# Performance work log

Hardware: AMD Instinct MI355X
Metric: run time of the kernel (lower is better)

Reference implementation:

```python
import jax, jax.numpy as jnp
import numpy as np

N = 4096
N_FEAT = 1024
N_HID = 8
N_HEADS = 8
N_CLASSES = 16
ALPHA = 0.2
NEG_BIG = -9e15


def setup_inputs() -> dict:
    key = jax.random.key(0)
    ks = jax.random.split(key, 6)
    x = jax.random.normal(ks[0], (N, N_FEAT), dtype=jnp.float32)
    adj = (jax.random.uniform(ks[1], (N, N)) < 0.01).astype(jnp.float32)
    adj = jnp.maximum(adj, jnp.eye(N, dtype=jnp.float32))
    W_heads = jax.random.normal(ks[2], (N_HEADS, N_FEAT, N_HID), dtype=jnp.float32) * 0.05
    a_heads = jax.random.normal(ks[3], (N_HEADS, 2 * N_HID, 1), dtype=jnp.float32) * 0.05
    W_final = jax.random.normal(ks[4], (N_HEADS * N_HID, N_CLASSES), dtype=jnp.float32) * 0.05
    a_final = jax.random.normal(ks[5], (2 * N_CLASSES, 1), dtype=jnp.float32) * 0.05
    return {"x": x, "adj": adj, "W_heads": W_heads, "a_heads": a_heads,
            "W_final": W_final, "a_final": a_final}


def gat_layer(h, adj, W, a):
    # h: [N, Fin], W: [Fin, Fout], a: [2*Fout, 1]
    Wh = h @ W                                  # [N, Fout]
    Fout = W.shape[1]
    f_src = Wh @ a[:Fout, 0]                    # [N] -- Wh_i . a[:F]
    f_dst = Wh @ a[Fout:, 0]                    # [N] -- Wh_j . a[F:]
    e = jax.nn.leaky_relu(f_src[:, None] + f_dst[None, :], ALPHA)  # [N, N]
    e = jnp.where(adj > 0, e, NEG_BIG)
    attention = jax.nn.softmax(e, axis=1)       # dropout skipped (eval mode)
    return attention @ Wh                        # [N, Fout]


def reference(x, adj, W_heads, a_heads, W_final, a_final):
    # multi-head GAT layer (8 independent heads), concat along features
    heads = jax.vmap(lambda W, a: gat_layer(x, adj, W, a))(W_heads, a_heads)  # [H, N, n_hid]
    h = jnp.transpose(heads, (1, 0, 2)).reshape(x.shape[0], -1)               # [N, H*n_hid]
    h = jax.nn.elu(h)
    out = gat_layer(h, adj, W_final, a_final)    # [N, n_classes]
    return jax.nn.log_softmax(out, axis=1)
```

## Files before the change

kernel.cpp:

```cpp
#include <hip/hip_runtime.h>
#include <math.h>

#define N 4096
#define NFEAT 1024
#define NHID 8
#define NHEADS 8
#define NCLS 16
#define CAP 128

#define GEMM_BLOCKS 512

__global__ __launch_bounds__(256) void ka_scan_gemm(const float* __restrict__ adj,
                                                    const float* __restrict__ x,
                                                    const float* __restrict__ W_heads,
                                                    const float* __restrict__ a_heads,
                                                    int* __restrict__ deg,
                                                    int* __restrict__ nbr,
                                                    float* __restrict__ Wh,
                                                    float* __restrict__ fsrc,
                                                    float* __restrict__ fdst) {
    __shared__ float smem[8 * NFEAT + 4 * 8 * 64];
    const int tid = threadIdx.x;

    if (blockIdx.x >= GEMM_BLOCKS) {
        const int row = blockIdx.x - GEMM_BLOCKS;
        int* cnt = (int*)smem;
        if (tid == 0) *cnt = 0;
        __syncthreads();
        const float4* arow = (const float4*)(adj + (size_t)row * N);
        int* outl = nbr + (size_t)row * CAP;
        float4 v[4];
        #pragma unroll
        for (int i = 0; i < 4; ++i) v[i] = arow[tid + i * 256];
        #pragma unroll
        for (int i = 0; i < 4; ++i) {
            const int b = (tid + i * 256) * 4;
            if (v[i].x > 0.f) { int p = atomicAdd(cnt, 1); if (p < CAP) outl[p] = b + 0; }
            if (v[i].y > 0.f) { int p = atomicAdd(cnt, 1); if (p < CAP) outl[p] = b + 1; }
            if (v[i].z > 0.f) { int p = atomicAdd(cnt, 1); if (p < CAP) outl[p] = b + 2; }
            if (v[i].w > 0.f) { int p = atomicAdd(cnt, 1); if (p < CAP) outl[p] = b + 3; }
        }
        __syncthreads();
        if (tid == 0) deg[row] = *cnt > CAP ? CAP : *cnt;
        return;
    }

    float* xs = smem;
    float (*red)[8][64] = (float (*)[8][64])(smem + 8 * NFEAT);
    const int w = tid >> 6, c = tid & 63;
    const int row0 = blockIdx.x * 8;

    const float4* xg = (const float4*)(x + (size_t)row0 * NFEAT);
    float4* xls = (float4*)xs;
    #pragma unroll
    for (int i = 0; i < 8; ++i) xls[tid + i * 256] = xg[tid + i * 256];
    __syncthreads();

    float acc[8] = {};
    const float* wp = W_heads + (size_t)(c >> 3) * (NFEAT * NHID) + (c & 7)
                    + (size_t)(w * 256) * NHID;
    const float* xw = xs + w * 256;
    for (int k = 0; k < 256; k += 8) {
        float wv[8];
        #pragma unroll
        for (int u = 0; u < 8; ++u) wv[u] = wp[(k + u) * 8];
        #pragma unroll
        for (int r = 0; r < 8; ++r) {
            const float4 a0 = *(const float4*)(xw + r * NFEAT + k);
            const float4 a1 = *(const float4*)(xw + r * NFEAT + k + 4);
            acc[r] += a0.x * wv[0] + a0.y * wv[1] + a0.z * wv[2] + a0.w * wv[3]
                    + a1.x * wv[4] + a1.y * wv[5] + a1.z * wv[6] + a1.w * wv[7];
        }
    }
    #pragma unroll
    for (int r = 0; r < 8; ++r) red[w][r][c] = acc[r];
    __syncthreads();
    #pragma unroll
    for (int e0 = 0; e0 < 2; ++e0) {
        int e = tid + e0 * 256;
        int r = e >> 6, cc = e & 63;
        float v = red[0][r][cc] + red[1][r][cc] + red[2][r][cc] + red[3][r][cc];
        Wh[(size_t)(row0 + r) * 64 + cc] = v;
        int h = cc >> 3, kh = cc & 7;
        float vs = v * a_heads[h * 16 + kh];
        float vd = v * a_heads[h * 16 + 8 + kh];
        vs += __shfl_xor(vs, 1); vs += __shfl_xor(vs, 2); vs += __shfl_xor(vs, 4);
        vd += __shfl_xor(vd, 1); vd += __shfl_xor(vd, 2); vd += __shfl_xor(vd, 4);
        if (kh == 0) { fsrc[h * N + row0 + r] = vs; fdst[h * N + row0 + r] = vd; }
    }
}

__global__ __launch_bounds__(256) void kb_attn1(const float* __restrict__ fsrc,
                                                const float* __restrict__ fdst,
                                                const float* __restrict__ Wh,
                                                const int* __restrict__ deg,
                                                const int* __restrict__ nbr,
                                                const float* __restrict__ W_final,
                                                const float* __restrict__ a_final,
                                                float* __restrict__ Wh2,
                                                float* __restrict__ fsrc2,
                                                float* __restrict__ fdst2) {
    __shared__ float hrow[4][64];
    const int wave = threadIdx.x >> 6;
    const int lane = threadIdx.x & 63;
    const int row = blockIdx.x * 4 + wave;
    const int h = lane >> 3;
    const int d = deg[row];
    const int* nl = nbr + (size_t)row * CAP;
    const float fs = fsrc[h * N + row];
    const float* fd = fdst + h * N;

    float s = 0.f, acc = 0.f;
    int n = 0;
    for (; n + 4 <= d; n += 4) {
        int j0 = nl[n], j1 = nl[n + 1], j2 = nl[n + 2], j3 = nl[n + 3];
        float e0 = fs + fd[j0], e1 = fs + fd[j1], e2 = fs + fd[j2], e3 = fs + fd[j3];
        float v0 = Wh[(size_t)j0 * 64 + lane], v1 = Wh[(size_t)j1 * 64 + lane];
        float v2 = Wh[(size_t)j2 * 64 + lane], v3 = Wh[(size_t)j3 * 64 + lane];
        float w0 = __expf(fmaxf(e0, 0.2f * e0));
        float w1 = __expf(fmaxf(e1, 0.2f * e1));
        float w2 = __expf(fmaxf(e2, 0.2f * e2));
        float w3 = __expf(fmaxf(e3, 0.2f * e3));
        s += (w0 + w1) + (w2 + w3);
        acc += w0 * v0 + w1 * v1 + w2 * v2 + w3 * v3;
    }
    for (; n < d; ++n) {
        int j = nl[n];
        float e = fs + fd[j];
        float wgt = __expf(fmaxf(e, 0.2f * e));
        s += wgt;
        acc += wgt * Wh[(size_t)j * 64 + lane];
    }
    float o = acc / s;
    o = o > 0.f ? o : (__expf(o) - 1.f);
    hrow[wave][lane] = o;
    __syncthreads();

    const int g = lane >> 4, cc = lane & 15;
    float p = 0.f;
    #pragma unroll
    for (int f0 = 0; f0 < 16; ++f0) {
        int f = g * 16 + f0;
        p += hrow[wave][f] * W_final[f * 16 + cc];
    }
    p += __shfl_xor(p, 16);
    p += __shfl_xor(p, 32);
    if (g == 0) Wh2[(size_t)row * 16 + cc] = p;
    float vs = p * a_final[cc];
    float vd = p * a_final[16 + cc];
    #pragma unroll
    for (int mm = 1; mm < 16; mm <<= 1) {
        vs += __shfl_xor(vs, mm);
        vd += __shfl_xor(vd, mm);
    }
    if (lane == 0) { fsrc2[row] = vs; fdst2[row] = vd; }
}

__global__ __launch_bounds__(256) void kc_attn2(const float* __restrict__ fsrc2,
                                                const float* __restrict__ fdst2,
                                                const float* __restrict__ Wh2,
                                                const int* __restrict__ deg,
                                                const int* __restrict__ nbr,
                                                float* __restrict__ out) {
    const int wave = threadIdx.x >> 6;
    const int lane = threadIdx.x & 63;
    const int row = blockIdx.x * 4 + wave;
    const int jj = lane >> 4, c = lane & 15;
    const int d = deg[row];
    const int* nl = nbr + (size_t)row * CAP;
    const float fs = fsrc2[row];

    float s = 0.f, acc = 0.f;
    for (int n = jj; n < d; n += 4) {
        int j = nl[n];
        float e = fs + fdst2[j];
        float w = __expf(fmaxf(e, 0.2f * e));
        s += w;
        acc += w * Wh2[(size_t)j * 16 + c];
    }
    s += __shfl_xor(s, 16);  s += __shfl_xor(s, 32);
    acc += __shfl_xor(acc, 16); acc += __shfl_xor(acc, 32);

    float u = acc / s;
    float m2 = u;
    #pragma unroll
    for (int mm = 1; mm < 16; mm <<= 1) m2 = fmaxf(m2, __shfl_xor(m2, mm));
    float tv = u - m2;
    float se = __expf(tv);
    #pragma unroll
    for (int mm = 1; mm < 16; mm <<= 1) se += __shfl_xor(se, mm);
    float o = tv - logf(se);
    if (jj == 0) out[(size_t)row * 16 + c] = o;
}

extern "C" void kernel_launch(void* const* d_in, const int* in_sizes, int n_in,
                              void* d_out, int out_size, void* d_ws, size_t ws_size,
                              hipStream_t stream) {
    const float* x       = (const float*)d_in[0];
    const float* adj     = (const float*)d_in[1];
    const float* W_heads = (const float*)d_in[2];
    const float* a_heads = (const float*)d_in[3];
    const float* W_final = (const float*)d_in[4];
    const float* a_final = (const float*)d_in[5];
    float* out = (float*)d_out;

    float* ws    = (float*)d_ws;
    float* Wh    = ws;
    float* fsrc  = Wh + 262144;
    float* fdst  = fsrc + 32768;
    float* Wh2   = fdst + 32768;
    float* fsrc2 = Wh2 + 65536;
    float* fdst2 = fsrc2 + 4096;
    int*   deg   = (int*)(fdst2 + 4096);
    int*   nbr   = deg + 4096;

    ka_scan_gemm<<<GEMM_BLOCKS + N, 256, 0, stream>>>(adj, x, W_heads, a_heads,
                                                      deg, nbr, Wh, fsrc, fdst);
    kb_attn1    <<<N / 4, 256, 0, stream>>>(fsrc, fdst, Wh, deg, nbr,
                                            W_final, a_final, Wh2, fsrc2, fdst2);
    kc_attn2    <<<N / 4, 256, 0, stream>>>(fsrc2, fdst2, Wh2, deg, nbr, out);
}
```

Before: 139.8 us.

## Parallelize neighbor aggregation across lanes with shuffle reductions in attention kernels

In the first attention kernel, each lane now handles one neighbor slot per head and computes that neighbor's attention weight once. It loads the head's eight features as float4 pairs and merges partial sums with a butterfly shuffle transpose, replacing the old scheme where every lane in a head group recomputed the weight. In the second kernel, all 64 lanes compute neighbor weights in parallel up front, and the aggregation loop broadcasts indices and weights with shuffles using two accumulators. This cuts redundant exp and gather work and shortens the serial dependency chains, at the cost of more shuffle instructions and an unrolled loop capped at 128 neighbors.

```diff
diff --git a/kernel.cpp b/kernel.cpp
--- a/kernel.cpp
+++ b/kernel.cpp
@@ -105,33 +105,47 @@
     const int lane = threadIdx.x & 63;
     const int row = blockIdx.x * 4 + wave;
     const int h = lane >> 3;
+    const int nn = lane & 7;
     const int d = deg[row];
     const int* nl = nbr + (size_t)row * CAP;
     const float fs = fsrc[h * N + row];
     const float* fd = fdst + h * N;
 
-    float s = 0.f, acc = 0.f;
-    int n = 0;
-    for (; n + 4 <= d; n += 4) {
-        int j0 = nl[n], j1 = nl[n + 1], j2 = nl[n + 2], j3 = nl[n + 3];
-        float e0 = fs + fd[j0], e1 = fs + fd[j1], e2 = fs + fd[j2], e3 = fs + fd[j3];
-        float v0 = Wh[(size_t)j0 * 64 + lane], v1 = Wh[(size_t)j1 * 64 + lane];
-        float v2 = Wh[(size_t)j2 * 64 + lane], v3 = Wh[(size_t)j3 * 64 + lane];
-        float w0 = __expf(fmaxf(e0, 0.2f * e0));
-        float w1 = __expf(fmaxf(e1, 0.2f * e1));
-        float w2 = __expf(fmaxf(e2, 0.2f * e2));
-        float w3 = __expf(fmaxf(e3, 0.2f * e3));
-        s += (w0 + w1) + (w2 + w3);
-        acc += w0 * v0 + w1 * v1 + w2 * v2 + w3 * v3;
-    }
-    for (; n < d; ++n) {
-        int j = nl[n];
-        float e = fs + fd[j];
-        float wgt = __expf(fmaxf(e, 0.2f * e));
-        s += wgt;
-        acc += wgt * Wh[(size_t)j * 64 + lane];
-    }
-    float o = acc / s;
+    float pacc[8] = {0.f, 0.f, 0.f, 0.f, 0.f, 0.f, 0.f, 0.f};
+    float sp = 0.f;
+
+    #pragma unroll
+    for (int r = 0; r < 16; ++r) {
+        if (r * 8 < d) {
+            const int n = r * 8 + nn;
+            const bool vv = n < d;
+            const int j = vv ? nl[n] : 0;
+            const float e = fs + fd[j];
+            const float w = vv ? __expf(fmaxf(e, 0.2f * e)) : 0.f;
+            sp += w;
+            const float4 wv0 = *(const float4*)(Wh + (size_t)j * 64 + h * 8);
+            const float4 wv1 = *(const float4*)(Wh + (size_t)j * 64 + h * 8 + 4);
+            pacc[0] += w * wv0.x; pacc[1] += w * wv0.y;
+            pacc[2] += w * wv0.z; pacc[3] += w * wv0.w;
+            pacc[4] += w * wv1.x; pacc[5] += w * wv1.y;
+            pacc[6] += w * wv1.z; pacc[7] += w * wv1.w;
+        }
+    }
+
+    sp += __shfl_xor(sp, 1);
+    sp += __shfl_xor(sp, 2);
+    sp += __shfl_xor(sp, 4);
+
+    const int k0 = nn & 1, k1 = (nn >> 1) & 1, k2 = nn >> 2;
+    float t0 = (k0 ? pacc[1] : pacc[0]) + __shfl_xor(k0 ? pacc[0] : pacc[1], 1);
+    float t1 = (k0 ? pacc[3] : pacc[2]) + __shfl_xor(k0 ? pacc[2] : pacc[3], 1);
+    float t2 = (k0 ? pacc[5] : pacc[4]) + __shfl_xor(k0 ? pacc[4] : pacc[5], 1);
+    float t3 = (k0 ? pacc[7] : pacc[6]) + __shfl_xor(k0 ? pacc[6] : pacc[7], 1);
+    float u0 = (k1 ? t1 : t0) + __shfl_xor(k1 ? t0 : t1, 2);
+    float u1 = (k1 ? t3 : t2) + __shfl_xor(k1 ? t2 : t3, 2);
+    float of = (k2 ? u1 : u0) + __shfl_xor(k2 ? u0 : u1, 4);
+
+    float o = of / sp;
     o = o > 0.f ? o : (__expf(o) - 1.f);
     hrow[wave][lane] = o;
     __syncthreads();
@@ -170,16 +184,51 @@
     const int* nl = nbr + (size_t)row * CAP;
     const float fs = fsrc2[row];
 
-    float s = 0.f, acc = 0.f;
-    for (int n = jj; n < d; n += 4) {
-        int j = nl[n];
-        float e = fs + fdst2[j];
-        float w = __expf(fmaxf(e, 0.2f * e));
-        s += w;
-        acc += w * Wh2[(size_t)j * 16 + c];
-    }
-    s += __shfl_xor(s, 16);  s += __shfl_xor(s, 32);
-    acc += __shfl_xor(acc, 16); acc += __shfl_xor(acc, 32);
+    const bool v0 = lane < d;
+    const int jl0 = v0 ? nl[lane] : 0;
+    const float e0 = fs + fdst2[jl0];
+    const float w0 = v0 ? __expf(fmaxf(e0, 0.2f * e0)) : 0.f;
+
+    int jl1 = 0;
+    float w1 = 0.f;
+    if (__builtin_expect(d > 64, 0)) {
+        const bool v1 = 64 + lane < d;
+        const int jx = v1 ? nl[64 + lane] : 0;
+        jl1 = jx;
+        const float e1 = fs + fdst2[jx];
+        w1 = v1 ? __expf(fmaxf(e1, 0.2f * e1)) : 0.f;
+    }
+
+    float s = w0 + w1;
+    #pragma unroll
+    for (int mm = 1; mm < 64; mm <<= 1) s += __shfl_xor(s, mm);
+
+    const int dc = d < 64 ? d : 64;
+    float acc = 0.f, acc2 = 0.f;
+    int n = jj;
+    for (; n + 4 < dc; n += 8) {
+        const int ja = __shfl(jl0, n);
+        const float wa = __shfl(w0, n);
+        const int jb = __shfl(jl0, n + 4);
+        const float wb = __shfl(w0, n + 4);
+        acc  += wa * Wh2[(size_t)ja * 16 + c];
+        acc2 += wb * Wh2[(size_t)jb * 16 + c];
+    }
+    if (n < dc) {
+        const int ja = __shfl(jl0, n);
+        const float wa = __shfl(w0, n);
+        acc += wa * Wh2[(size_t)ja * 16 + c];
+    }
+    if (__builtin_expect(d > 64, 0)) {
+        for (int m = 64 + jj; m < d; m += 4) {
+            const int jb = __shfl(jl1, m - 64);
+            const float wb = __shfl(w1, m - 64);
+            acc2 += wb * Wh2[(size_t)jb * 16 + c];
+        }
+    }
+    acc += acc2;
+    acc += __shfl_xor(acc, 16);
+    acc += __shfl_xor(acc, 32);
 
     float u = acc / s;
     float m2 = u;
```

Measured after the change: 135.4 us. 1.03x faster.
